# Optimization experiments

Hardware: AMD Instinct MI355X
Metric: run time of the kernel (lower is better)

The kernel has to match this reference:

```python
import jax, jax.numpy as jnp
import numpy as np
import math

B, ENC, SEQ, H = 32, 512, 1024, 8
HD = SEQ // H  # 128
EPS = 1e-5


def setup_inputs() -> dict:
    key = jax.random.key(0)
    ks = jax.random.split(key, 7)
    s = 0.02
    return {
        "x": jax.random.normal(ks[0], (B, ENC, SEQ), jnp.float32),
        "ln_g": jnp.ones((SEQ,), jnp.float32),
        "ln_b": jnp.zeros((SEQ,), jnp.float32),
        "w_in": jax.random.normal(ks[1], (3 * SEQ, SEQ), jnp.float32) * s,
        "b_in": jnp.zeros((3 * SEQ,), jnp.float32),
        "w_m1a": jax.random.normal(ks[2], (HD, HD), jnp.float32) * s,
        "b_m1a": jnp.zeros((HD,), jnp.float32),
        "w_m1b": jax.random.normal(ks[3], (1, HD), jnp.float32) * s,
        "b_m1b": jnp.zeros((1,), jnp.float32),
        "w_m2": jax.random.normal(ks[4], (1, ENC), jnp.float32) * s,
        "b_m2": jnp.zeros((1,), jnp.float32),
        "w_out": jax.random.normal(ks[5], (SEQ, 2 * SEQ), jnp.float32) * s,
        "b_out": jnp.zeros((SEQ,), jnp.float32),
    }


def reference(x, ln_g, ln_b, w_in, b_in, w_m1a, b_m1a, w_m1b, b_m1b,
              w_m2, b_m2, w_out, b_out):
    Bsz, N, S = x.shape  # N == enc_in, S == seq_len == d_model
    hd = S // H
    scale = 1.0 / math.sqrt(hd * N)

    # LayerNorm over last dim
    mu = jnp.mean(x, axis=-1, keepdims=True)
    var = jnp.mean(jnp.square(x - mu), axis=-1, keepdims=True)
    xn = (x - mu) * jax.lax.rsqrt(var + EPS) * ln_g + ln_b

    qkv = xn @ w_in.T + b_in  # [B, N, 3S]
    q, k, v = jnp.split(qkv, 3, axis=-1)
    # torch .view(B, H, N, hd) on contiguous [B, N, S] is a raw reshape
    q = q.reshape(Bsz, H, N, hd)
    k = k.reshape(Bsz, H, N, hd)
    v = v.reshape(Bsz, H, N, hd)

    def mlp1(t):  # [B,H,N,hd] -> [B,H,N]
        h1 = jnp.maximum(jnp.einsum('bhnd,ed->bhne', t, w_m1a) + b_m1a, 0.0)
        return jnp.einsum('bhne,e->bhn', h1, w_m1b[0]) + b_m1b[0]

    def mlp2(t):  # [B,H,N,hd] -> [B,H,hd] (Linear over N then ReLU)
        return jnp.maximum(jnp.einsum('bhnd,n->bhd', t, w_m2[0]) + b_m2[0], 0.0)

    # rank-1 outer-product scores, broadcast-multiplied into v
    s_qk = mlp1(q)[..., None] * mlp2(k)[:, :, None, :] * scale  # [B,H,N,hd]
    v1 = (s_qk * v).reshape(Bsz, N, S)
    s_kq = mlp1(k)[..., None] * mlp2(q)[:, :, None, :] * scale
    v2 = (s_kq * v).reshape(Bsz, N, S)

    out = jnp.concatenate([v1, v2], axis=-1) @ w_out.T + b_out  # [B,N,S]
    return out + x  # dropout is identity at eval
```

## Files before the change

kernel.cpp:

```cpp
#include <hip/hip_runtime.h>
#include <hip/hip_fp8.h>
#include <cstdint>
#include <cstddef>

#define BSZ   32
#define ENCN  512
#define SEQL  1024
#define MROWS (BSZ*ENCN)
#define N1    (3*SEQL)
#define K1    SEQL
#define N2    SEQL
#define K2    (2*SEQL)

typedef __bf16 bf16;
typedef float  f32x4  __attribute__((ext_vector_type(4)));
typedef int    i32x4  __attribute__((ext_vector_type(4)));
typedef int    i32x8  __attribute__((ext_vector_type(8)));

__device__ __forceinline__ void gl_lds16(const void* g, void* l) {
  __builtin_amdgcn_global_load_lds(
      (const __attribute__((address_space(1))) void*)(uintptr_t)g,
      (__attribute__((address_space(3))) void*)(uintptr_t)(uint32_t)(uintptr_t)l,
      16, 0, 0);
}

__device__ __forceinline__ uint32_t pk4_fp8(float a, float b, float c, float d) {
  int v = __builtin_amdgcn_cvt_pk_fp8_f32(a, b, 0, false);
  v = __builtin_amdgcn_cvt_pk_fp8_f32(c, d, v, true);
  return (uint32_t)v;
}
__device__ __forceinline__ uint8_t pk1_fp8(float a) {
  return (uint8_t)(__builtin_amdgcn_cvt_pk_fp8_f32(a, a, 0, false) & 0xff);
}
__device__ __forceinline__ float fp8_to_f(uint32_t b) {
  __hip_fp8_e4m3 t; t.__x = (__hip_fp8_storage_t)b; return (float)t;
}

__device__ __forceinline__ f32x4 mfma8(long a, long b, f32x4 c) {
  return __builtin_amdgcn_mfma_f32_16x16x32_fp8_fp8(a, b, c, 0, 0, 0);
}

__global__ __launch_bounds__(256) void cvt_w_kernel(const float* __restrict__ w_in,
                                                    const float* __restrict__ w_out,
                                                    const float* __restrict__ w1a,
                                                    uint8_t* __restrict__ wi8,
                                                    uint8_t* __restrict__ wo8,
                                                    uint8_t* __restrict__ w1a8) {
  int idx = blockIdx.x * 256 + threadIdx.x;
  const int NWIN4 = (N1 * K1) / 4;
  const int NOUT4 = (N2 * K2) / 4;
  const float4* src;
  uint32_t* dst;
  int j;
  if (idx < NWIN4) {
    src = (const float4*)w_in;  dst = (uint32_t*)wi8;  j = idx;
  } else if (idx < NWIN4 + NOUT4) {
    src = (const float4*)w_out; dst = (uint32_t*)wo8;  j = idx - NWIN4;
  } else {
    src = (const float4*)w1a;   dst = (uint32_t*)w1a8; j = idx - NWIN4 - NOUT4;
  }
  float4 v = src[j];
  dst[j] = pk4_fp8(v.x * 64.f, v.y * 64.f, v.z * 64.f, v.w * 64.f);
}

__global__ __launch_bounds__(256) void ln_kernel(const float* __restrict__ x,
                                                 const float* __restrict__ g,
                                                 const float* __restrict__ bt,
                                                 uint8_t* __restrict__ xn8) {
  int row = blockIdx.x;
  int t = threadIdx.x;
  const float4 v = ((const float4*)(x + (size_t)row * SEQL))[t];
  float s  = v.x + v.y + v.z + v.w;
  float ss = v.x*v.x + v.y*v.y + v.z*v.z + v.w*v.w;
  for (int off = 32; off; off >>= 1) {
    s  += __shfl_down(s,  off, 64);
    ss += __shfl_down(ss, off, 64);
  }
  __shared__ float red[8];
  int w = t >> 6, l = t & 63;
  if (l == 0) { red[w] = s; red[w + 4] = ss; }
  __syncthreads();
  float st  = red[0] + red[1] + red[2] + red[3];
  float sst = red[4] + red[5] + red[6] + red[7];
  float mu   = st * (1.0f / SEQL);
  float var  = sst * (1.0f / SEQL) - mu * mu;
  float rstd = rsqrtf(var + 1e-5f);
  float4 gv = ((const float4*)g)[t];
  float4 bv = ((const float4*)bt)[t];
  float y0 = (v.x - mu) * rstd * gv.x + bv.x;
  float y1 = (v.y - mu) * rstd * gv.y + bv.y;
  float y2 = (v.z - mu) * rstd * gv.z + bv.z;
  float y3 = (v.w - mu) * rstd * gv.w + bv.w;
  ((uint32_t*)(xn8 + (size_t)row * SEQL))[t] = pk4_fp8(y0, y1, y2, y3);
}

template <int MODE, int SA, int SB>
__device__ __forceinline__ void gemm_fp8_impl(const uint8_t* __restrict__ A,
                                              const uint8_t* __restrict__ Bw,
                                              const float* __restrict__ bias,
                                              const float* __restrict__ resid,
                                              void* __restrict__ Cout,
                                              int M, int N, int K) {
  __shared__ uint8_t Als[128 * 128];
  __shared__ uint8_t Bls[128 * 128];
  const int tid = threadIdx.x;
  const int w = tid >> 6, l = tid & 63;
  const int wm = w & 1, wn = w >> 1;
  const int q = l >> 4, li = l & 15;
  const int m0 = blockIdx.x * 128;
  const int n0 = blockIdx.y * 128;

  const int srow = tid >> 3;
  const int scol = ((tid & 7) ^ (srow & 7)) << 4;

  const int c0 = ((2 * q)     ^ (li & 7)) << 4;
  const int c1 = ((2 * q + 1) ^ (li & 7)) << 4;

  f32x4 acc[4][4] = {};

  for (int k0 = 0; k0 < K; k0 += 128) {
#pragma unroll
    for (int is = 0; is < 4; is++) {
      gl_lds16(A  + (size_t)(m0 + is * 32 + srow) * K + k0 + scol,
               (char*)Als + is * 4096 + w * 1024);
      gl_lds16(Bw + (size_t)(n0 + is * 32 + srow) * K + k0 + scol,
               (char*)Bls + is * 4096 + w * 1024);
    }
    __syncthreads();
    i32x8 af[4], bfg[4];
#pragma unroll
    for (int i = 0; i < 4; i++) {
      int r = wm * 64 + i * 16 + li;
      i32x4 lo = *(const i32x4*)&Als[r * 128 + c0];
      i32x4 hi = *(const i32x4*)&Als[r * 128 + c1];
      af[i] = i32x8{lo[0], lo[1], lo[2], lo[3], hi[0], hi[1], hi[2], hi[3]};
    }
#pragma unroll
    for (int j = 0; j < 4; j++) {
      int r = wn * 64 + j * 16 + li;
      i32x4 lo = *(const i32x4*)&Bls[r * 128 + c0];
      i32x4 hi = *(const i32x4*)&Bls[r * 128 + c1];
      bfg[j] = i32x8{lo[0], lo[1], lo[2], lo[3], hi[0], hi[1], hi[2], hi[3]};
    }
#pragma unroll
    for (int i = 0; i < 4; i++)
#pragma unroll
      for (int j = 0; j < 4; j++)
        acc[i][j] = __builtin_amdgcn_mfma_scale_f32_16x16x128_f8f6f4(
            af[i], bfg[j], acc[i][j], 0 , 0 ,
            0, SA, 0, SB);
    __syncthreads();
  }

#pragma unroll
  for (int i = 0; i < 4; i++)
#pragma unroll
    for (int j = 0; j < 4; j++) {
      int col = n0 + wn * 64 + j * 16 + li;
      float bv = bias[col];
#pragma unroll
      for (int r = 0; r < 4; r++) {
        int row = m0 + wm * 64 + i * 16 + q * 4 + r;
        float v = acc[i][j][r] + bv;
        if (MODE == 0) {
          ((uint8_t*)Cout)[(size_t)row * N + col] = pk1_fp8(v * 64.f);
        } else {
          ((float*)Cout)[(size_t)row * N + col] = v + resid[(size_t)row * N + col];
        }
      }
    }
}

__global__ __launch_bounds__(256) void gemm_qkv(const uint8_t* __restrict__ A,
                                                const uint8_t* __restrict__ Bw,
                                                const float* __restrict__ bias,
                                                uint8_t* __restrict__ Cout) {
  gemm_fp8_impl<0, 127, 121>(A, Bw, bias, nullptr, Cout, MROWS, N1, K1);
}
__global__ __launch_bounds__(256) void gemm_out(const uint8_t* __restrict__ A,
                                                const uint8_t* __restrict__ Bw,
                                                const float* __restrict__ bias,
                                                const float* __restrict__ resid,
                                                float* __restrict__ Cout) {
  gemm_fp8_impl<1, 113, 121>(A, Bw, bias, resid, Cout, MROWS, N2, K2);
}

__global__ __launch_bounds__(256) void mlp12_kernel(const uint8_t* __restrict__ qkv8,
                                                    const uint8_t* __restrict__ w1a8,
                                                    const float* __restrict__ b1a,
                                                    const float* __restrict__ w1b,
                                                    const float* __restrict__ b1b,
                                                    const float* __restrict__ w2,
                                                    float* __restrict__ A1q,
                                                    float* __restrict__ A1k,
                                                    float* __restrict__ A2p) {
  __shared__ float red1[2][128];
  __shared__ float redm[16][128];
  __shared__ float w2s[128];
  const int bid = blockIdx.x;
  const int T = bid >> 10;
  const int rem = bid & 1023;
  const int bh = rem >> 2, quarter = rem & 3;
  const int tid = threadIdx.x;
  const int w = tid >> 6, l = tid & 63;
  const int wm = w & 1, wn = w >> 1;
  const int q = l >> 4, li = l & 15;
  const int R0 = bh * 64 + quarter * 16;
  const uint8_t* rbase = qkv8 + (size_t)R0 * N1 + T * 1024;

  if (tid < 128) w2s[tid] = w2[quarter * 128 + tid];

  long bfrag[4][4];
  float b1av[4], w1bv[4];
#pragma unroll
  for (int j = 0; j < 4; j++) {
    int n = wn * 64 + j * 16 + li;
#pragma unroll
    for (int kq = 0; kq < 4; kq++)
      bfrag[kq][j] = *(const long*)&w1a8[n * 128 + kq * 32 + q * 8];
    b1av[j] = b1a[n];
    w1bv[j] = w1b[n];
  }

  f32x4 acc[4][4] = {};
#pragma unroll
  for (int kq = 0; kq < 4; kq++) {
#pragma unroll
    for (int i = 0; i < 4; i++) {
      int lc = wm * 64 + i * 16 + li;
      long af = *(const long*)(rbase + (size_t)(lc >> 3) * N1
                               + (lc & 7) * 128 + kq * 32 + q * 8);
#pragma unroll
      for (int j = 0; j < 4; j++)
        acc[i][j] = mfma8(af, bfrag[kq][j], acc[i][j]);
    }
  }
  const float inv4096 = 1.0f / 4096.0f;
#pragma unroll
  for (int i = 0; i < 4; i++)
#pragma unroll
    for (int r = 0; r < 4; r++) {
      float s = 0.f;
#pragma unroll
      for (int j = 0; j < 4; j++)
        s += fmaxf(acc[i][j][r] * inv4096 + b1av[j], 0.f) * w1bv[j];
      for (int off = 1; off < 16; off <<= 1) s += __shfl_xor(s, off, 64);
      if (li == 0) red1[wn][wm * 64 + i * 16 + q * 4 + r] = s;
    }
  __syncthreads();
  if (tid < 128) {
    float v = red1[0][tid] + red1[1][tid] + b1b[0];
    (T ? A1k : A1q)[bh * 512 + quarter * 128 + tid] = v;
  }

  const int rg = tid >> 4, dg = tid & 15;
  const uint8_t* arow = rbase + (size_t)rg * N1 + dg * 8;
  float a8[8] = {0, 0, 0, 0, 0, 0, 0, 0};
#pragma unroll
  for (int cc = 0; cc < 8; cc++) {
    uint64_t vb = *(const uint64_t*)(arow + cc * 128);
    float wgt = w2s[rg * 8 + cc];
#pragma unroll
    for (int e = 0; e < 8; e++)
      a8[e] += fp8_to_f((uint32_t)(vb >> (8 * e)) & 0xff) * wgt;
  }
#pragma unroll
  for (int e = 0; e < 8; e++) redm[rg][dg * 8 + e] = a8[e];
  __syncthreads();
  if (tid < 128) {
    float s = 0.f;
#pragma unroll
    for (int rg2 = 0; rg2 < 16; rg2++) s += redm[rg2][tid];
    A2p[(((size_t)T * 256 + bh) * 4 + quarter) * 128 + tid] = s;
  }
}

__global__ __launch_bounds__(256) void a2c_kernel(const float* __restrict__ A2p,
                                                  const float* __restrict__ b2,
                                                  float* __restrict__ A2q,
                                                  float* __restrict__ A2k) {
  int idx = blockIdx.x * 256 + threadIdx.x;
  int t = idx >> 15, r = idx & 32767;
  int bh = r >> 7, d = r & 127;
  const float* p = A2p + ((size_t)t * 256 + bh) * 512 + d;
  float s = (p[0] + p[128] + p[256] + p[384]) * (1.0f / 64.0f) + b2[0];
  (t ? A2k : A2q)[r] = fmaxf(s, 0.f);
}

__global__ __launch_bounds__(256) void scale_kernel(const uint8_t* __restrict__ qkv8,
                                                    const float* __restrict__ A1q,
                                                    const float* __restrict__ A1k,
                                                    const float* __restrict__ A2q,
                                                    const float* __restrict__ A2k,
                                                    uint8_t* __restrict__ Y) {
  size_t idx = ((size_t)blockIdx.x * 256 + threadIdx.x) * 8;
  int b = (int)(idx >> 19);
  int f = (int)(idx & 524287);
  int chunk = f >> 7;
  float a1q = A1q[b * 4096 + chunk];
  float a1k = A1k[b * 4096 + chunk];
  int a2i = b * 1024 + ((f >> 16) << 7) + (f & 127);
  float4 k0 = *(const float4*)&A2k[a2i];
  float4 k1 = *(const float4*)&A2k[a2i + 4];
  float4 q0 = *(const float4*)&A2q[a2i];
  float4 q1 = *(const float4*)&A2q[a2i + 4];
  int row = b * 512 + (f >> 10);
  int col = f & 1023;
  uint64_t vb = *(const uint64_t*)(qkv8 + (size_t)row * N1 + 2048 + col);
  float kk[8] = { k0.x, k0.y, k0.z, k0.w, k1.x, k1.y, k1.z, k1.w };
  float qq[8] = { q0.x, q0.y, q0.z, q0.w, q1.x, q1.y, q1.z, q1.w };
  float y1[8], y2[8];
#pragma unroll
  for (int e = 0; e < 8; e++) {
    float v64 = fp8_to_f((uint32_t)(vb >> (8 * e)) & 0xff);
    y1[e] = a1q * kk[e] * v64;
    y2[e] = a1k * qq[e] * v64;
  }
  uint8_t* yr = Y + (size_t)row * K2;
  ((uint32_t*)(yr + col))[0] = pk4_fp8(y1[0], y1[1], y1[2], y1[3]);
  ((uint32_t*)(yr + col))[1] = pk4_fp8(y1[4], y1[5], y1[6], y1[7]);
  ((uint32_t*)(yr + 1024 + col))[0] = pk4_fp8(y2[0], y2[1], y2[2], y2[3]);
  ((uint32_t*)(yr + 1024 + col))[1] = pk4_fp8(y2[4], y2[5], y2[6], y2[7]);
}

extern "C" void kernel_launch(void* const* d_in, const int* in_sizes, int n_in,
                              void* d_out, int out_size, void* d_ws, size_t ws_size,
                              hipStream_t stream) {
  const float* x     = (const float*)d_in[0];
  const float* ln_g  = (const float*)d_in[1];
  const float* ln_b  = (const float*)d_in[2];
  const float* w_in  = (const float*)d_in[3];
  const float* b_in  = (const float*)d_in[4];
  const float* w1a   = (const float*)d_in[5];
  const float* b1a   = (const float*)d_in[6];
  const float* w1b   = (const float*)d_in[7];
  const float* b1b   = (const float*)d_in[8];
  const float* w2    = (const float*)d_in[9];
  const float* b2    = (const float*)d_in[10];
  const float* w_out = (const float*)d_in[11];
  const float* b_out = (const float*)d_in[12];
  float* out = (float*)d_out;
  char* ws = (char*)d_ws;

  uint8_t* xn8  = (uint8_t*)(ws);
  uint8_t* Y8   = (uint8_t*)(ws);
  uint8_t* qkv8 = (uint8_t*)(ws + 33554432);
  uint8_t* wi8  = (uint8_t*)(ws + 83886080);
  uint8_t* wo8  = (uint8_t*)(ws + 87031808);
  uint8_t* w1a8 = (uint8_t*)(ws + 89128960);
  float*   A1q  = (float*)  (ws + 89145344);
  float*   A1k  = (float*)  (ws + 89669632);
  float*   A2p  = (float*)  (ws + 90193920);
  float*   A2q  = (float*)  (ws + 91242496);
  float*   A2k  = (float*)  (ws + 91373568);

  cvt_w_kernel<<<5136, 256, 0, stream>>>(w_in, w_out, w1a, wi8, wo8, w1a8);
  ln_kernel<<<MROWS, 256, 0, stream>>>(x, ln_g, ln_b, xn8);
  gemm_qkv<<<dim3(MROWS / 128, N1 / 128), 256, 0, stream>>>(xn8, wi8, b_in, qkv8);
  mlp12_kernel<<<2048, 256, 0, stream>>>(qkv8, w1a8, b1a, w1b, b1b, w2, A1q, A1k, A2p);
  a2c_kernel<<<256, 256, 0, stream>>>(A2p, b2, A2q, A2k);
  scale_kernel<<<8192, 256, 0, stream>>>(qkv8, A1q, A1k, A2q, A2k, Y8);
  gemm_out<<<dim3(MROWS / 128, N2 / 128), 256, 0, stream>>>(Y8, wo8, b_out, x, out);
}
```

Baseline: 325.9 us.

## Stage GEMM epilogue through LDS for vectorized stores; widen MLP1 fragment loads

New measurement: 312.9 us. 4.0% less time.

```diff
diff --git a/kernel.cpp b/kernel.cpp
--- a/kernel.cpp
+++ b/kernel.cpp
@@ -16,6 +16,7 @@
 typedef float  f32x4  __attribute__((ext_vector_type(4)));
 typedef int    i32x4  __attribute__((ext_vector_type(4)));
 typedef int    i32x8  __attribute__((ext_vector_type(8)));
+typedef long   i64x2  __attribute__((ext_vector_type(2)));
 
 __device__ __forceinline__ void gl_lds16(const void* g, void* l) {
   __builtin_amdgcn_global_load_lds(
@@ -28,9 +29,6 @@
   int v = __builtin_amdgcn_cvt_pk_fp8_f32(a, b, 0, false);
   v = __builtin_amdgcn_cvt_pk_fp8_f32(c, d, v, true);
   return (uint32_t)v;
-}
-__device__ __forceinline__ uint8_t pk1_fp8(float a) {
-  return (uint8_t)(__builtin_amdgcn_cvt_pk_fp8_f32(a, a, 0, false) & 0xff);
 }
 __device__ __forceinline__ float fp8_to_f(uint32_t b) {
   __hip_fp8_e4m3 t; t.__x = (__hip_fp8_storage_t)b; return (float)t;
@@ -101,8 +99,9 @@
                                               const float* __restrict__ resid,
                                               void* __restrict__ Cout,
                                               int M, int N, int K) {
-  __shared__ uint8_t Als[128 * 128];
-  __shared__ uint8_t Bls[128 * 128];
+  __shared__ __align__(16) uint8_t smem[32768];
+  uint8_t* Als = smem;
+  uint8_t* Bls = smem + 16384;
   const int tid = threadIdx.x;
   const int w = tid >> 6, l = tid & 63;
   const int wm = w & 1, wn = w >> 1;
@@ -152,23 +151,50 @@
     __syncthreads();
   }
 
-#pragma unroll
-  for (int i = 0; i < 4; i++)
-#pragma unroll
-    for (int j = 0; j < 4; j++) {
-      int col = n0 + wn * 64 + j * 16 + li;
-      float bv = bias[col];
-#pragma unroll
-      for (int r = 0; r < 4; r++) {
-        int row = m0 + wm * 64 + i * 16 + q * 4 + r;
-        float v = acc[i][j][r] + bv;
-        if (MODE == 0) {
-          ((uint8_t*)Cout)[(size_t)row * N + col] = pk1_fp8(v * 64.f);
-        } else {
-          ((float*)Cout)[(size_t)row * N + col] = v + resid[(size_t)row * N + col];
-        }
+  float* Wf = (float*)smem + w * 1088;
+#pragma unroll
+  for (int i = 0; i < 4; i++) {
+#pragma unroll
+    for (int j = 0; j < 4; j++)
+#pragma unroll
+      for (int r = 0; r < 4; r++)
+        Wf[(q * 4 + r) * 68 + j * 16 + li] = acc[i][j][r];
+    __syncthreads();
+    const int row = m0 + wm * 64 + i * 16 + li;
+    if (MODE == 0) {
+      const int cb = n0 + wn * 64 + q * 16;
+      f32x4 v0 = *(const f32x4*)&Wf[li * 68 + q * 16 + 0];
+      f32x4 v1 = *(const f32x4*)&Wf[li * 68 + q * 16 + 4];
+      f32x4 v2 = *(const f32x4*)&Wf[li * 68 + q * 16 + 8];
+      f32x4 v3 = *(const f32x4*)&Wf[li * 68 + q * 16 + 12];
+      float4 b0 = *(const float4*)&bias[cb + 0];
+      float4 b1 = *(const float4*)&bias[cb + 4];
+      float4 b2 = *(const float4*)&bias[cb + 8];
+      float4 b3 = *(const float4*)&bias[cb + 12];
+      i32x4 d;
+      d[0] = (int)pk4_fp8((v0[0]+b0.x)*64.f, (v0[1]+b0.y)*64.f,
+                          (v0[2]+b0.z)*64.f, (v0[3]+b0.w)*64.f);
+      d[1] = (int)pk4_fp8((v1[0]+b1.x)*64.f, (v1[1]+b1.y)*64.f,
+                          (v1[2]+b1.z)*64.f, (v1[3]+b1.w)*64.f);
+      d[2] = (int)pk4_fp8((v2[0]+b2.x)*64.f, (v2[1]+b2.y)*64.f,
+                          (v2[2]+b2.z)*64.f, (v2[3]+b2.w)*64.f);
+      d[3] = (int)pk4_fp8((v3[0]+b3.x)*64.f, (v3[1]+b3.y)*64.f,
+                          (v3[2]+b3.z)*64.f, (v3[3]+b3.w)*64.f);
+      *(i32x4*)((uint8_t*)Cout + (size_t)row * N + cb) = d;
+    } else {
+#pragma unroll
+      for (int c4 = 0; c4 < 4; c4++) {
+        const int cb = n0 + wn * 64 + c4 * 16 + q * 4;
+        f32x4 vv = *(const f32x4*)&Wf[li * 68 + c4 * 16 + q * 4];
+        float4 bb = *(const float4*)&bias[cb];
+        float4 rr = *(const float4*)&resid[(size_t)row * N + cb];
+        float4 o = { vv[0] + bb.x + rr.x, vv[1] + bb.y + rr.y,
+                     vv[2] + bb.z + rr.z, vv[3] + bb.w + rr.w };
+        *(float4*)((float*)Cout + (size_t)row * N + cb) = o;
       }
     }
+    __syncthreads();
+  }
 }
 
 __global__ __launch_bounds__(256) void gemm_qkv(const uint8_t* __restrict__ A,
@@ -217,23 +243,24 @@
     int n = wn * 64 + j * 16 + li;
 #pragma unroll
     for (int kq = 0; kq < 4; kq++)
-      bfrag[kq][j] = *(const long*)&w1a8[n * 128 + kq * 32 + q * 8];
+      bfrag[kq][j] = *(const long*)&w1a8[n * 128 + q * 32 + kq * 8];
     b1av[j] = b1a[n];
     w1bv[j] = w1b[n];
   }
 
   f32x4 acc[4][4] = {};
 #pragma unroll
-  for (int kq = 0; kq < 4; kq++) {
-#pragma unroll
-    for (int i = 0; i < 4; i++) {
-      int lc = wm * 64 + i * 16 + li;
-      long af = *(const long*)(rbase + (size_t)(lc >> 3) * N1
-                               + (lc & 7) * 128 + kq * 32 + q * 8);
+  for (int i = 0; i < 4; i++) {
+    int lc = wm * 64 + i * 16 + li;
+    const uint8_t* abase = rbase + (size_t)(lc >> 3) * N1 + (lc & 7) * 128 + q * 32;
+    i64x2 p0 = *(const i64x2*)abase;
+    i64x2 p1 = *(const i64x2*)(abase + 16);
+    long f[4] = { p0[0], p0[1], p1[0], p1[1] };
+#pragma unroll
+    for (int kq = 0; kq < 4; kq++)
 #pragma unroll
       for (int j = 0; j < 4; j++)
-        acc[i][j] = mfma8(af, bfrag[kq][j], acc[i][j]);
-    }
+        acc[i][j] = mfma8(f[kq], bfrag[kq][j], acc[i][j]);
   }
   const float inv4096 = 1.0f / 4096.0f;
 #pragma unroll
```
